# Kernel tuning notes

Measured on AMD Instinct MI355X. Metric: run time of the kernel, lower is better.

Reference implementation:

```python
import jax, jax.numpy as jnp
import numpy as np

B, S, D, C = 1024, 200, 64, 256  # batch, max_seq_length_all, reshape_size, codebook_size


def setup_inputs() -> dict:
    key = jax.random.key(0)
    k1, k2, k3 = jax.random.split(key, 3)
    rq_item_embeddings = jax.random.normal(k1, (B, S, D), dtype=jnp.float32)
    labels = jax.random.randint(k2, (B, S), 0, C, dtype=jnp.int32)
    attention_mask = jax.random.randint(k3, (B, S), 0, 2, dtype=jnp.int32)
    return {
        "rq_item_embeddings": rq_item_embeddings,
        "labels": labels,
        "attention_mask": attention_mask,
    }


def reference(rq_item_embeddings, labels, attention_mask):
    # Batched version of the original per-sample loop:
    #   M[c, s] = 1 if labels[s] == c, masked by attention_mask[s]
    #   M <- L1-normalize over seq dim (divide each cluster row by its count)
    #   cluster_emb = M @ sample  (per-cluster mean of item embeddings)
    x = rq_item_embeddings  # [B, S, D]
    mask = attention_mask.astype(x.dtype)  # [B, S]
    # one-hot cluster assignment, [B, C, S]
    one_hot = (labels[:, None, :] == jnp.arange(C, dtype=labels.dtype)[None, :, None])
    cluster_mask = one_hot.astype(x.dtype) * mask[:, None, :]  # [B, C, S]
    counts = cluster_mask.sum(axis=-1)  # [B, C]  (== L1 norm of each row)
    inv = jnp.where(counts > 0, 1.0 / jnp.maximum(counts, 1.0), 0.0)  # [B, C]
    # normalized scatter matrix @ embeddings -> per-cluster mean, [B, C, D]
    cluster_emb = jnp.einsum('bcs,bsd->bcd', cluster_mask, x) * inv[:, :, None]
    return cluster_emb, cluster_mask.astype(jnp.int32)
```

## Files before the change

### kernel.cpp

```cpp
#include <hip/hip_runtime.h>

#define NB 1024
#define NS 200
#define ND 64
#define NC 256

typedef float v4f __attribute__((ext_vector_type(4)));

__global__ __launch_bounds__(256, 8) void s3rec_cluster_kernel(
    const float* __restrict__ x,
    const int*   __restrict__ labels,
    const int*   __restrict__ amask,
    float* __restrict__ out_emb,
    float* __restrict__ out_mask)
{
    __shared__ __align__(16) int s_lab[NS];
    __shared__ int   s_cnt[NC];
    __shared__ int   s_off[NC];
    __shared__ float s_inv[NC];
    __shared__ int   s_list[NS];
    __shared__ int   s_part[4];

    const int role = blockIdx.x % 3;
    const int b    = blockIdx.x / 3;
    const int t    = threadIdx.x;

    for (int i = t; i < NS; i += 256) {
        const int l = labels[b * NS + i];
        const int m = amask [b * NS + i];
        s_lab[i] = (m != 0) ? l : -1;
    }

    if (role < 2) {
        __syncthreads();
        v4f* om4 = reinterpret_cast<v4f*>(out_mask + (size_t)b * (NC * NS));
        const int i4lo = role * 6400;
        #pragma unroll 5
        for (int k = 0; k < 25; ++k) {
            const int i4 = i4lo + k * 256 + t;
            const int c  = i4 / 50;
            const int s0 = (i4 - c * 50) * 4;
            const int4 lv = *reinterpret_cast<const int4*>(&s_lab[s0]);
            v4f v;
            v.x = (lv.x == c) ? 1.0f : 0.0f;
            v.y = (lv.y == c) ? 1.0f : 0.0f;
            v.z = (lv.z == c) ? 1.0f : 0.0f;
            v.w = (lv.w == c) ? 1.0f : 0.0f;
            om4[i4] = v;
        }
        return;
    }

    s_cnt[t] = 0;
    __syncthreads();
    if (t < NS) {
        const int l = s_lab[t];
        if (l >= 0) atomicAdd(&s_cnt[l], 1);
    }
    __syncthreads();

    const int lane = t & 63;
    const int w    = t >> 6;
    const int cnt  = s_cnt[t];
    s_inv[t] = (cnt > 0) ? (1.0f / (float)cnt) : 0.0f;

    int v = cnt;
    #pragma unroll
    for (int d = 1; d < 64; d <<= 1) {
        const int n = __shfl_up(v, d, 64);
        if (lane >= d) v += n;
    }
    if (lane == 63) s_part[w] = v;
    __syncthreads();
    int base = 0;
    for (int i = 0; i < w; ++i) base += s_part[i];
    s_off[t] = base + v - cnt;
    __syncthreads();

    if (t < NS) {
        const int L = s_lab[t];
        if (L >= 0) {
            int r = 0;
            for (int s2 = 0; s2 < t; ++s2) r += (s_lab[s2] == L) ? 1 : 0;
            s_list[s_off[L] + r] = t;
        }
    }
    __syncthreads();

    const float* xb = x + (size_t)b * NS * ND;
    float* oe = out_emb + (size_t)b * (NC * ND);
    for (int cc = 0; cc < 64; cc += 2) {
        const int c0 = w * 64 + cc;
        const int c1 = c0 + 1;
        const int n0 = s_cnt[c0], o0 = s_off[c0];
        const int n1 = s_cnt[c1], o1 = s_off[c1];
        float a0 = 0.0f, a1 = 0.0f;
        const int nm = (n0 > n1) ? n0 : n1;
        for (int j = 0; j < nm; ++j) {
            if (j < n0) a0 += xb[s_list[o0 + j] * ND + lane];
            if (j < n1) a1 += xb[s_list[o1 + j] * ND + lane];
        }
        oe[c0 * ND + lane] = a0 * s_inv[c0];
        oe[c1 * ND + lane] = a1 * s_inv[c1];
    }
}

extern "C" void kernel_launch(void* const* d_in, const int* in_sizes, int n_in,
                              void* d_out, int out_size, void* d_ws, size_t ws_size,
                              hipStream_t stream) {
    const float* x      = (const float*)d_in[0];
    const int*   labels = (const int*)  d_in[1];
    const int*   amask  = (const int*)  d_in[2];

    float* out_emb  = (float*)d_out;
    float* out_mask = out_emb + (size_t)NB * NC * ND;

    s3rec_cluster_kernel<<<dim3(NB * 3), dim3(256), 0, stream>>>(
        x, labels, amask, out_emb, out_mask);
}
```

Baseline: 326.8 us.

## Merge mask-writer and gather roles into two symmetric blocks per batch

```diff
diff --git a/kernel.cpp b/kernel.cpp
--- a/kernel.cpp
+++ b/kernel.cpp
@@ -7,7 +7,7 @@
 
 typedef float v4f __attribute__((ext_vector_type(4)));
 
-__global__ __launch_bounds__(256, 8) void s3rec_cluster_kernel(
+__global__ __launch_bounds__(256, 4) void s3rec_cluster_kernel(
     const float* __restrict__ x,
     const int*   __restrict__ labels,
     const int*   __restrict__ amask,
@@ -21,38 +21,18 @@
     __shared__ int   s_list[NS];
     __shared__ int   s_part[4];
 
-    const int role = blockIdx.x % 3;
-    const int b    = blockIdx.x / 3;
+    const int half = blockIdx.x & 1;
+    const int b    = blockIdx.x >> 1;
     const int t    = threadIdx.x;
 
-    for (int i = t; i < NS; i += 256) {
-        const int l = labels[b * NS + i];
-        const int m = amask [b * NS + i];
-        s_lab[i] = (m != 0) ? l : -1;
+    if (t < NS) {
+        const int l = labels[b * NS + t];
+        const int m = amask [b * NS + t];
+        s_lab[t] = (m != 0) ? l : -1;
     }
-
-    if (role < 2) {
-        __syncthreads();
-        v4f* om4 = reinterpret_cast<v4f*>(out_mask + (size_t)b * (NC * NS));
-        const int i4lo = role * 6400;
-        #pragma unroll 5
-        for (int k = 0; k < 25; ++k) {
-            const int i4 = i4lo + k * 256 + t;
-            const int c  = i4 / 50;
-            const int s0 = (i4 - c * 50) * 4;
-            const int4 lv = *reinterpret_cast<const int4*>(&s_lab[s0]);
-            v4f v;
-            v.x = (lv.x == c) ? 1.0f : 0.0f;
-            v.y = (lv.y == c) ? 1.0f : 0.0f;
-            v.z = (lv.z == c) ? 1.0f : 0.0f;
-            v.w = (lv.w == c) ? 1.0f : 0.0f;
-            om4[i4] = v;
-        }
-        return;
-    }
-
     s_cnt[t] = 0;
     __syncthreads();
+
     if (t < NS) {
         const int l = s_lab[t];
         if (l >= 0) atomicAdd(&s_cnt[l], 1);
@@ -87,21 +67,46 @@
     }
     __syncthreads();
 
+    v4f* om4 = reinterpret_cast<v4f*>(out_mask + (size_t)b * (NC * NS));
+    const int i4lo = half * 6400;
+    #pragma unroll 5
+    for (int k = 0; k < 25; ++k) {
+        const int i4 = i4lo + k * 256 + t;
+        const int c  = i4 / 50;
+        const int s0 = (i4 - c * 50) * 4;
+        const int4 lv = *reinterpret_cast<const int4*>(&s_lab[s0]);
+        v4f mv;
+        mv.x = (lv.x == c) ? 1.0f : 0.0f;
+        mv.y = (lv.y == c) ? 1.0f : 0.0f;
+        mv.z = (lv.z == c) ? 1.0f : 0.0f;
+        mv.w = (lv.w == c) ? 1.0f : 0.0f;
+        om4[i4] = mv;
+    }
+
     const float* xb = x + (size_t)b * NS * ND;
     float* oe = out_emb + (size_t)b * (NC * ND);
-    for (int cc = 0; cc < 64; cc += 2) {
-        const int c0 = w * 64 + cc;
-        const int c1 = c0 + 1;
-        const int n0 = s_cnt[c0], o0 = s_off[c0];
-        const int n1 = s_cnt[c1], o1 = s_off[c1];
-        float a0 = 0.0f, a1 = 0.0f;
-        const int nm = (n0 > n1) ? n0 : n1;
+    const int cbase = half * 128 + w * 32;
+    for (int cc = 0; cc < 32; cc += 4) {
+        const int c0 = cbase + cc;
+        const int n0 = s_cnt[c0 + 0], o0 = s_off[c0 + 0];
+        const int n1 = s_cnt[c0 + 1], o1 = s_off[c0 + 1];
+        const int n2 = s_cnt[c0 + 2], o2 = s_off[c0 + 2];
+        const int n3 = s_cnt[c0 + 3], o3 = s_off[c0 + 3];
+        float a0 = 0.0f, a1 = 0.0f, a2 = 0.0f, a3 = 0.0f;
+        int nm = n0;
+        nm = (n1 > nm) ? n1 : nm;
+        nm = (n2 > nm) ? n2 : nm;
+        nm = (n3 > nm) ? n3 : nm;
         for (int j = 0; j < nm; ++j) {
             if (j < n0) a0 += xb[s_list[o0 + j] * ND + lane];
             if (j < n1) a1 += xb[s_list[o1 + j] * ND + lane];
+            if (j < n2) a2 += xb[s_list[o2 + j] * ND + lane];
+            if (j < n3) a3 += xb[s_list[o3 + j] * ND + lane];
         }
-        oe[c0 * ND + lane] = a0 * s_inv[c0];
-        oe[c1 * ND + lane] = a1 * s_inv[c1];
+        oe[(c0 + 0) * ND + lane] = a0 * s_inv[c0 + 0];
+        oe[(c0 + 1) * ND + lane] = a1 * s_inv[c0 + 1];
+        oe[(c0 + 2) * ND + lane] = a2 * s_inv[c0 + 2];
+        oe[(c0 + 3) * ND + lane] = a3 * s_inv[c0 + 3];
     }
 }
 
@@ -115,6 +120,6 @@
     float* out_emb  = (float*)d_out;
     float* out_mask = out_emb + (size_t)NB * NC * ND;
 
-    s3rec_cluster_kernel<<<dim3(NB * 3), dim3(256), 0, stream>>>(
+    s3rec_cluster_kernel<<<dim3(NB * 2), dim3(256), 0, stream>>>(
         x, labels, amask, out_emb, out_mask);
 }
```

Measured after the change: 321.0 us. About the same (-1.8%).
